# Kernel optimization log

Hardware: AMD Instinct MI355X
Metric: run time of the kernel (lower is better)

The kernel has to match this reference:

```python
import jax, jax.numpy as jnp
import numpy as np

DIM = 256
NUM_HEADS = 8
HEAD_DIM = DIM // NUM_HEADS
WH, WW = 7, 7
N = WH * WW              # tokens per window = 49
NUM_WINDOWS = 64         # windows per image (56x56 map / 7x7 windows)
B_TOTAL = 2048           # num_windows * B_images
SCALE = HEAD_DIM ** -0.5


def _relative_position_index():
    # Matches the tf.meshgrid (xy indexing) construction in the source.
    coords = np.stack(np.meshgrid(np.arange(WH), np.arange(WW)), axis=0)  # [2, WW, WH]
    flat = coords.reshape(2, -1)                                          # [2, N]
    rel = flat[:, :, None] - flat[:, None, :]                             # [2, N, N]
    rel = rel.transpose(1, 2, 0).astype(np.int32)                         # [N, N, 2]
    rel[:, :, 0] += WH - 1
    rel[:, :, 1] += WW - 1
    rel[:, :, 0] *= 2 * WW - 1
    return rel.sum(-1)                                                    # [N, N]


def setup_inputs() -> dict:
    key = jax.random.key(0)
    ks = jax.random.split(key, 6)
    std = 0.02
    x = jax.random.normal(ks[0], (B_TOTAL, N, DIM), dtype=jnp.float32)
    mask = jnp.zeros((NUM_WINDOWS, N, N), dtype=jnp.float32)  # 0 / -inf additive mask
    qkv_w = jax.random.normal(ks[1], (DIM, 3 * DIM), dtype=jnp.float32) * std
    qkv_b = jnp.zeros((3 * DIM,), dtype=jnp.float32)
    proj_w = jax.random.normal(ks[2], (DIM, DIM), dtype=jnp.float32) * std
    proj_b = jnp.zeros((DIM,), dtype=jnp.float32)
    n_rel = (2 * WH - 1) * (2 * WW - 1)  # 169
    bias_table = jax.random.normal(ks[3], (n_rel, NUM_HEADS), dtype=jnp.float32) * std
    rel_index = jnp.asarray(_relative_position_index(), dtype=jnp.int32)
    return {"x": x, "mask": mask, "qkv_w": qkv_w, "qkv_b": qkv_b,
            "proj_w": proj_w, "proj_b": proj_b, "bias_table": bias_table,
            "rel_index": rel_index}


def reference(x, mask, qkv_w, qkv_b, proj_w, proj_b, bias_table, rel_index):
    B = x.shape[0]
    # qkv projection -> [3, B, H, N, hd]
    qkv = x @ qkv_w + qkv_b                                  # [B, N, 3C]
    qkv = qkv.reshape(B, N, 3, NUM_HEADS, HEAD_DIM)
    qkv = jnp.transpose(qkv, (2, 0, 3, 1, 4))
    q, k, v = qkv[0], qkv[1], qkv[2]
    # scaled attention scores [B, H, N, N]
    attn = jnp.einsum('bhnd,bhmd->bhnm', q, k) * SCALE
    # relative position bias gather: [N*N] -> [N, N, H] -> [1, H, N, N]
    bias = bias_table[rel_index.reshape(-1)].reshape(N, N, NUM_HEADS)
    attn = attn + jnp.transpose(bias, (2, 0, 1))[None]
    # additive window mask [nW, N, N]
    nW = mask.shape[0]
    attn = attn.reshape(B // nW, nW, NUM_HEADS, N, N) + mask[None, :, None]
    attn = attn.reshape(B, NUM_HEADS, N, N)
    attn = jax.nn.softmax(attn, axis=-1)
    out = jnp.einsum('bhnm,bhmd->bhnd', attn, v)             # [B, H, N, hd]
    out = jnp.transpose(out, (0, 2, 1, 3)).reshape(B, N, DIM)
    return out @ proj_w + proj_b
```

## Files before the change

### kernel.cpp

```cpp
#include <hip/hip_runtime.h>

#define NTOK 49
#define NHEAD 8
#define HDIM 32
#define DIMC 256
#define SCALE_F 0.17677669529663687f

typedef __attribute__((ext_vector_type(8))) short short8;
typedef __attribute__((ext_vector_type(4))) float f32x4;

#define AS1P(p) ((__attribute__((address_space(1))) void*)(p))
#define AS3P(p) ((__attribute__((address_space(3))) void*)(p))

__device__ inline unsigned short f2bf(float f) {
    unsigned int u = __float_as_uint(f);
    u += 0x7fffu + ((u >> 16) & 1u);
    return (unsigned short)(u >> 16);
}

__global__ __launch_bounds__(256) void conv_pack(const float* __restrict__ in,
    unsigned short* __restrict__ xp, int M)
{
    const int m  = blockIdx.x * 256 + threadIdx.x;
    const int kc = blockIdx.y;
    if (m >= M) return;
    const float4* p = (const float4*)(in + (size_t)m * 256 + kc * 8);
    float4 a = p[0], b = p[1];
    union { unsigned short s[8]; uint4 v; } u;
    u.s[0] = f2bf(a.x); u.s[1] = f2bf(a.y); u.s[2] = f2bf(a.z); u.s[3] = f2bf(a.w);
    u.s[4] = f2bf(b.x); u.s[5] = f2bf(b.y); u.s[6] = f2bf(b.z); u.s[7] = f2bf(b.w);
    *(uint4*)(xp + ((size_t)kc * M + m) * 8) = u.v;
}

__global__ __launch_bounds__(256) void pack_w(const float* __restrict__ W,
    unsigned short* __restrict__ Wp, int K, int N)
{
    int idx = blockIdx.x * 256 + threadIdx.x;
    if (idx >= K * N) return;
    int k = idx / N, n = idx - k * N;
    Wp[((size_t)(k >> 3) * N + n) * 8 + (k & 7)] = f2bf(W[idx]);
}

__global__ __launch_bounds__(256) void bm_build(const float* __restrict__ bias_table,
    const int* __restrict__ rel_index, const float* __restrict__ mask,
    float* __restrict__ bm)
{
    int idx = blockIdx.x * 256 + threadIdx.x;
    if (idx >= 64 * NHEAD * NTOK * NTOK) return;
    int wh = idx / (NTOK * NTOK);
    int ij = idx - wh * (NTOK * NTOK);
    int w = wh >> 3, h = wh & 7;
    bm[idx] = bias_table[rel_index[ij] * NHEAD + h] + mask[(size_t)w * (NTOK * NTOK) + ij];
}

template <bool OUT_BF16>
__global__ __launch_bounds__(256) void gemm_mfma(
    const unsigned short* __restrict__ Ap,
    const unsigned short* __restrict__ Wp,
    const float* __restrict__ Bv,
    void* __restrict__ Yv,
    int N, int M, int nbm)
{
    __shared__ __align__(16) unsigned short As[4096];
    __shared__ __align__(16) unsigned short Bs[4096];

    const int tid  = threadIdx.x;
    const int lane = tid & 63;
    const int wv   = tid >> 6;
    const int quad = lane >> 4;
    const int l15  = lane & 15;

    const int nbn = N >> 7;
    const int lin = blockIdx.x;
    int mblk, nblk;
    if ((nbm & 7) == 0) {
        const int xcd = lin & 7;
        const int g   = lin >> 3;
        const int gm  = g / nbn;
        mblk = xcd * (nbm >> 3) + gm;
        nblk = g - gm * nbn;
    } else {
        mblk = lin / nbn;
        nblk = lin - mblk * nbn;
    }
    const long m0 = (long)mblk * 128;
    const int  n0 = nblk * 128;
    const int  wm = (wv >> 1) * 64;
    const int  wn = (wv & 1) * 64;

    const unsigned short* ga0 = Ap + ((size_t)wv * M + m0 + lane) * 8;
    const unsigned short* ga1 = ga0 + 64 * 8;
    const unsigned short* gb0 = Wp + ((size_t)wv * N + n0 + lane) * 8;
    const unsigned short* gb1 = gb0 + 64 * 8;

    f32x4 acc[4][4];
    #pragma unroll
    for (int i = 0; i < 4; ++i)
        #pragma unroll
        for (int j = 0; j < 4; ++j) acc[i][j] = (f32x4){0.f, 0.f, 0.f, 0.f};

    for (int k0 = 0; k0 < 256; k0 += 32) {
        const size_t aofs = (size_t)(k0 >> 3) * M * 8;
        const size_t bofs = (size_t)(k0 >> 3) * N * 8;
        __builtin_amdgcn_global_load_lds(AS1P(ga0 + aofs), AS3P(As + wv * 1024),       16, 0, 0);
        __builtin_amdgcn_global_load_lds(AS1P(ga1 + aofs), AS3P(As + wv * 1024 + 512), 16, 0, 0);
        __builtin_amdgcn_global_load_lds(AS1P(gb0 + bofs), AS3P(Bs + wv * 1024),       16, 0, 0);
        __builtin_amdgcn_global_load_lds(AS1P(gb1 + bofs), AS3P(Bs + wv * 1024 + 512), 16, 0, 0);
        __syncthreads();
        short8 af[4], bq[4];
        #pragma unroll
        for (int t = 0; t < 4; ++t) {
            af[t] = *(const short8*)(As + quad * 1024 + (wm + t * 16 + l15) * 8);
            bq[t] = *(const short8*)(Bs + quad * 1024 + (wn + t * 16 + l15) * 8);
        }
        #pragma unroll
        for (int ti = 0; ti < 4; ++ti)
            #pragma unroll
            for (int tj = 0; tj < 4; ++tj)
                acc[ti][tj] = __builtin_amdgcn_mfma_f32_16x16x32_bf16(bq[tj], af[ti], acc[ti][tj], 0, 0, 0);
        __syncthreads();
    }

    float4 bv4[4];
    #pragma unroll
    for (int tj = 0; tj < 4; ++tj)
        bv4[tj] = *(const float4*)(Bv + n0 + wn + tj * 16 + quad * 4);

    #pragma unroll
    for (int ti = 0; ti < 4; ++ti) {
        const long row = m0 + wm + ti * 16 + l15;
        #pragma unroll
        for (int tj = 0; tj < 4; ++tj) {
            const int col = n0 + wn + tj * 16 + quad * 4;
            const float v0 = acc[ti][tj][0] + bv4[tj].x;
            const float v1 = acc[ti][tj][1] + bv4[tj].y;
            const float v2 = acc[ti][tj][2] + bv4[tj].z;
            const float v3 = acc[ti][tj][3] + bv4[tj].w;
            if (OUT_BF16) {
                uint2 u;
                u.x = (unsigned int)f2bf(v0) | ((unsigned int)f2bf(v1) << 16);
                u.y = (unsigned int)f2bf(v2) | ((unsigned int)f2bf(v3) << 16);
                *(uint2*)((unsigned short*)Yv + row * N + col) = u;
            } else {
                float4 o = {v0, v1, v2, v3};
                *(float4*)((float*)Yv + row * N + col) = o;
            }
        }
    }
}

__global__ __launch_bounds__(128) void attn_mfma(
    const unsigned short* __restrict__ qkvb,
    const float* __restrict__ bm,
    unsigned short* __restrict__ o1b,
    int win0, int Mc)
{
    __shared__ __align__(16) unsigned short SMEM[2 * 3528];

    const int wvid = threadIdx.x >> 6;
    const int lane = threadIdx.x & 63;
    const int h    = blockIdx.x * 2 + wvid;
    const int b    = blockIdx.y;
    const int w    = (win0 + b) & 63;
    const int quad = lane >> 4;
    const int l15  = lane & 15;

    unsigned short* Vt = SMEM + wvid * 3528;
    unsigned short* Ps = SMEM + wvid * 3528;

    const unsigned short* wbase = qkvb + (size_t)b * NTOK * 768 + h * HDIM;

    {
        const int tok = (lane < NTOK) ? lane : (NTOK - 1);
        const unsigned short* vp = wbase + (size_t)tok * 768 + 512;
        #pragma unroll
        for (int c = 0; c < 4; ++c) {
            uint4 vv = *(const uint4*)(vp + c * 8);
            unsigned int uu[4] = {vv.x, vv.y, vv.z, vv.w};
            #pragma unroll
            for (int e = 0; e < 4; ++e) {
                int d = c * 8 + e * 2;
                Vt[d * 72 + lane]       = (unsigned short)(uu[e] & 0xffffu);
                Vt[(d + 1) * 72 + lane] = (unsigned short)(uu[e] >> 16);
            }
        }
    }

    short8 aq[4], bk[4];
    #pragma unroll
    for (int t = 0; t < 4; ++t) {
        int row = t * 16 + l15; if (row >= NTOK) row = NTOK - 1;
        const unsigned short* rp = wbase + (size_t)row * 768 + quad * 8;
        aq[t] = *(const short8*)(rp);
        bk[t] = *(const short8*)(rp + 256);
    }

    f32x4 sa[4][4];
    #pragma unroll
    for (int ti = 0; ti < 4; ++ti)
        #pragma unroll
        for (int tj = 0; tj < 4; ++tj) {
            f32x4 z = (f32x4){0.f, 0.f, 0.f, 0.f};
            sa[ti][tj] = __builtin_amdgcn_mfma_f32_16x16x32_bf16(aq[ti], bk[tj], z, 0, 0, 0);
        }

    short8 vb2[2][2];
    #pragma unroll
    for (int td = 0; td < 2; ++td)
        #pragma unroll
        for (int kc = 0; kc < 2; ++kc)
            vb2[td][kc] = *(const short8*)(Vt + (td * 16 + l15) * 72 + kc * 32 + quad * 8);

    const float* bmb = bm + (size_t)(w * NHEAD + h) * (NTOK * NTOK);
    float inv[4][4];
    #pragma unroll
    for (int ti = 0; ti < 4; ++ti) {
        #pragma unroll
        for (int r = 0; r < 4; ++r) {
            const int row = ti * 16 + quad * 4 + r;
            float sv[4];
            #pragma unroll
            for (int tj = 0; tj < 4; ++tj) {
                const int col = tj * 16 + l15;
                float s;
                if (col < NTOK) {
                    float add = (row < NTOK) ? bmb[row * NTOK + col] : 0.f;
                    s = sa[ti][tj][r] * SCALE_F + add;
                } else {
                    s = -__builtin_inff();
                }
                sv[tj] = s;
            }
            float mx = fmaxf(fmaxf(sv[0], sv[1]), fmaxf(sv[2], sv[3]));
            mx = fmaxf(mx, __shfl_xor(mx, 1, 16));
            mx = fmaxf(mx, __shfl_xor(mx, 2, 16));
            mx = fmaxf(mx, __shfl_xor(mx, 4, 16));
            mx = fmaxf(mx, __shfl_xor(mx, 8, 16));
            float e0 = __expf(sv[0] - mx), e1 = __expf(sv[1] - mx);
            float e2 = __expf(sv[2] - mx), e3 = __expf(sv[3] - mx);
            sa[ti][0][r] = e0; sa[ti][1][r] = e1; sa[ti][2][r] = e2; sa[ti][3][r] = e3;
            float sum = (e0 + e1) + (e2 + e3);
            sum += __shfl_xor(sum, 1, 16);
            sum += __shfl_xor(sum, 2, 16);
            sum += __shfl_xor(sum, 4, 16);
            sum += __shfl_xor(sum, 8, 16);
            inv[ti][r] = 1.f / sum;
        }
    }

    __syncthreads();

    #pragma unroll
    for (int ti = 0; ti < 4; ++ti)
        #pragma unroll
        for (int r = 0; r < 4; ++r) {
            const int row = ti * 16 + quad * 4 + r;
            if (row < NTOK) {
                #pragma unroll
                for (int tj = 0; tj < 4; ++tj)
                    Ps[row * 72 + tj * 16 + l15] = f2bf(sa[ti][tj][r]);
            }
        }

    short8 pa[4][2];
    #pragma unroll
    for (int ti = 0; ti < 4; ++ti) {
        int row = ti * 16 + l15; if (row >= NTOK) row = NTOK - 1;
        #pragma unroll
        for (int kc = 0; kc < 2; ++kc)
            pa[ti][kc] = *(const short8*)(Ps + row * 72 + kc * 32 + quad * 8);
    }
    f32x4 oa[4][2];
    #pragma unroll
    for (int ti = 0; ti < 4; ++ti)
        #pragma unroll
        for (int td = 0; td < 2; ++td) {
            f32x4 z = (f32x4){0.f, 0.f, 0.f, 0.f};
            z = __builtin_amdgcn_mfma_f32_16x16x32_bf16(pa[ti][0], vb2[td][0], z, 0, 0, 0);
            oa[ti][td] = __builtin_amdgcn_mfma_f32_16x16x32_bf16(pa[ti][1], vb2[td][1], z, 0, 0, 0);
        }

    #pragma unroll
    for (int ti = 0; ti < 4; ++ti)
        #pragma unroll
        for (int r = 0; r < 4; ++r) {
            const int row = ti * 16 + quad * 4 + r;
            if (row < NTOK) {
                const float si = inv[ti][r];
                const size_t gm = (size_t)b * NTOK + row;
                #pragma unroll
                for (int td = 0; td < 2; ++td) {
                    const int kk = h * HDIM + td * 16 + l15;
                    o1b[((size_t)(kk >> 3) * Mc + gm) * 8 + (kk & 7)] = f2bf(oa[ti][td][r] * si);
                }
            }
        }
}

extern "C" void kernel_launch(void* const* d_in, const int* in_sizes, int n_in,
                              void* d_out, int out_size, void* d_ws, size_t ws_size,
                              hipStream_t stream)
{
    const float* x          = (const float*)d_in[0];
    const float* mask       = (const float*)d_in[1];
    const float* qkv_w      = (const float*)d_in[2];
    const float* qkv_b      = (const float*)d_in[3];
    const float* proj_w     = (const float*)d_in[4];
    const float* proj_b     = (const float*)d_in[5];
    const float* bias_table = (const float*)d_in[6];
    const int*   rel_index  = (const int*)d_in[7];
    float* outp = (float*)d_out;

    const int B_TOTAL = 2048;
    char* ws = (char*)d_ws;
    size_t off = 0;
    auto carve = [&](size_t bytes) -> void* {
        void* p = ws + off; off += (bytes + 255) & ~(size_t)255; return p;
    };
    unsigned short* WpQ = (unsigned short*)carve((size_t)256 * 768 * 2);
    unsigned short* WpP = (unsigned short*)carve((size_t)256 * 256 * 2);
    float* bm = (float*)carve((size_t)64 * NHEAD * NTOK * NTOK * 4);
    const size_t fixed = off;
    const size_t PER_WIN = (size_t)NTOK * 256 * 2 + (size_t)NTOK * 768 * 2 + (size_t)NTOK * 256 * 2;
    size_t avail = (ws_size > fixed + 1024) ? (ws_size - fixed - 1024) : 0;
    int chunkW = (int)(avail / PER_WIN);
    if (chunkW > B_TOTAL) chunkW = B_TOTAL;
    chunkW &= ~127;
    if (chunkW < 128) chunkW = 128;
    unsigned short* x_bf = (unsigned short*)carve((size_t)chunkW * NTOK * 256 * 2);
    unsigned short* qkvb = (unsigned short*)carve((size_t)chunkW * NTOK * 768 * 2);
    unsigned short* o1b  = (unsigned short*)carve((size_t)chunkW * NTOK * 256 * 2);

    pack_w<<<(256 * 768 + 255) / 256, 256, 0, stream>>>(qkv_w, WpQ, 256, 768);
    pack_w<<<(256 * 256 + 255) / 256, 256, 0, stream>>>(proj_w, WpP, 256, 256);
    bm_build<<<(64 * NHEAD * NTOK * NTOK + 255) / 256, 256, 0, stream>>>(
        bias_table, rel_index, mask, bm);

    for (int w0 = 0; w0 < B_TOTAL; w0 += chunkW) {
        int wc = B_TOTAL - w0; if (wc > chunkW) wc = chunkW;
        const int Mc = wc * NTOK;
        const int nbm = Mc / 128;
        conv_pack<<<dim3((Mc + 255) / 256, 32), 256, 0, stream>>>(
            x + (size_t)w0 * NTOK * DIMC, x_bf, Mc);
        gemm_mfma<true ><<<dim3(nbm * 6), 256, 0, stream>>>(x_bf, WpQ, qkv_b, qkvb, 768, Mc, nbm);
        attn_mfma<<<dim3(NHEAD / 2, wc), 128, 0, stream>>>(qkvb, bm, o1b, w0, Mc);
        gemm_mfma<false><<<dim3(nbm * 2), 256, 0, stream>>>(
            o1b, WpP, proj_b, outp + (size_t)w0 * NTOK * DIMC, 256, Mc, nbm);
    }
}
```

Baseline: 413.9 us.

## Fuse fp32-to-bf16 input conversion into QKV GEMM and coalesce attention output stores

```diff
diff --git a/kernel.cpp b/kernel.cpp
--- a/kernel.cpp
+++ b/kernel.cpp
@@ -16,20 +16,6 @@
     unsigned int u = __float_as_uint(f);
     u += 0x7fffu + ((u >> 16) & 1u);
     return (unsigned short)(u >> 16);
-}
-
-__global__ __launch_bounds__(256) void conv_pack(const float* __restrict__ in,
-    unsigned short* __restrict__ xp, int M)
-{
-    const int m  = blockIdx.x * 256 + threadIdx.x;
-    const int kc = blockIdx.y;
-    if (m >= M) return;
-    const float4* p = (const float4*)(in + (size_t)m * 256 + kc * 8);
-    float4 a = p[0], b = p[1];
-    union { unsigned short s[8]; uint4 v; } u;
-    u.s[0] = f2bf(a.x); u.s[1] = f2bf(a.y); u.s[2] = f2bf(a.z); u.s[3] = f2bf(a.w);
-    u.s[4] = f2bf(b.x); u.s[5] = f2bf(b.y); u.s[6] = f2bf(b.z); u.s[7] = f2bf(b.w);
-    *(uint4*)(xp + ((size_t)kc * M + m) * 8) = u.v;
 }
 
 __global__ __launch_bounds__(256) void pack_w(const float* __restrict__ W,
@@ -53,9 +39,9 @@
     bm[idx] = bias_table[rel_index[ij] * NHEAD + h] + mask[(size_t)w * (NTOK * NTOK) + ij];
 }
 
-template <bool OUT_BF16>
+template <bool A_F32, bool OUT_BF16>
 __global__ __launch_bounds__(256) void gemm_mfma(
-    const unsigned short* __restrict__ Ap,
+    const void* __restrict__ Av,
     const unsigned short* __restrict__ Wp,
     const float* __restrict__ Bv,
     void* __restrict__ Yv,
@@ -88,11 +74,21 @@
     const int  wm = (wv >> 1) * 64;
     const int  wn = (wv & 1) * 64;
 
-    const unsigned short* ga0 = Ap + ((size_t)wv * M + m0 + lane) * 8;
-    const unsigned short* ga1 = ga0 + 64 * 8;
     const unsigned short* gb0 = Wp + ((size_t)wv * N + n0 + lane) * 8;
     const unsigned short* gb1 = gb0 + 64 * 8;
 
+    const float* xr0 = nullptr;
+    const float* xr1 = nullptr;
+    const unsigned short* ga0 = nullptr;
+    const unsigned short* ga1 = nullptr;
+    if constexpr (A_F32) {
+        xr0 = (const float*)Av + (size_t)(m0 + lane) * 256 + wv * 8;
+        xr1 = xr0 + (size_t)64 * 256;
+    } else {
+        ga0 = (const unsigned short*)Av + ((size_t)wv * M + m0 + lane) * 8;
+        ga1 = ga0 + 64 * 8;
+    }
+
     f32x4 acc[4][4];
     #pragma unroll
     for (int i = 0; i < 4; ++i)
@@ -100,12 +96,28 @@
         for (int j = 0; j < 4; ++j) acc[i][j] = (f32x4){0.f, 0.f, 0.f, 0.f};
 
     for (int k0 = 0; k0 < 256; k0 += 32) {
-        const size_t aofs = (size_t)(k0 >> 3) * M * 8;
         const size_t bofs = (size_t)(k0 >> 3) * N * 8;
-        __builtin_amdgcn_global_load_lds(AS1P(ga0 + aofs), AS3P(As + wv * 1024),       16, 0, 0);
-        __builtin_amdgcn_global_load_lds(AS1P(ga1 + aofs), AS3P(As + wv * 1024 + 512), 16, 0, 0);
-        __builtin_amdgcn_global_load_lds(AS1P(gb0 + bofs), AS3P(Bs + wv * 1024),       16, 0, 0);
-        __builtin_amdgcn_global_load_lds(AS1P(gb1 + bofs), AS3P(Bs + wv * 1024 + 512), 16, 0, 0);
+        if constexpr (A_F32) {
+            float4 a0 = ((const float4*)(xr0 + k0))[0];
+            float4 a1 = ((const float4*)(xr0 + k0))[1];
+            float4 a2 = ((const float4*)(xr1 + k0))[0];
+            float4 a3 = ((const float4*)(xr1 + k0))[1];
+            __builtin_amdgcn_global_load_lds(AS1P(gb0 + bofs), AS3P(Bs + wv * 1024),       16, 0, 0);
+            __builtin_amdgcn_global_load_lds(AS1P(gb1 + bofs), AS3P(Bs + wv * 1024 + 512), 16, 0, 0);
+            union { unsigned short s[8]; uint4 v; } u0, u1;
+            u0.s[0] = f2bf(a0.x); u0.s[1] = f2bf(a0.y); u0.s[2] = f2bf(a0.z); u0.s[3] = f2bf(a0.w);
+            u0.s[4] = f2bf(a1.x); u0.s[5] = f2bf(a1.y); u0.s[6] = f2bf(a1.z); u0.s[7] = f2bf(a1.w);
+            u1.s[0] = f2bf(a2.x); u1.s[1] = f2bf(a2.y); u1.s[2] = f2bf(a2.z); u1.s[3] = f2bf(a2.w);
+            u1.s[4] = f2bf(a3.x); u1.s[5] = f2bf(a3.y); u1.s[6] = f2bf(a3.z); u1.s[7] = f2bf(a3.w);
+            *(uint4*)(As + wv * 1024 + (size_t)lane * 8)        = u0.v;
+            *(uint4*)(As + wv * 1024 + (size_t)(64 + lane) * 8) = u1.v;
+        } else {
+            const size_t aofs = (size_t)(k0 >> 3) * M * 8;
+            __builtin_amdgcn_global_load_lds(AS1P(ga0 + aofs), AS3P(As + wv * 1024),       16, 0, 0);
+            __builtin_amdgcn_global_load_lds(AS1P(ga1 + aofs), AS3P(As + wv * 1024 + 512), 16, 0, 0);
+            __builtin_amdgcn_global_load_lds(AS1P(gb0 + bofs), AS3P(Bs + wv * 1024),       16, 0, 0);
+            __builtin_amdgcn_global_load_lds(AS1P(gb1 + bofs), AS3P(Bs + wv * 1024 + 512), 16, 0, 0);
+        }
         __syncthreads();
         short8 af[4], bq[4];
         #pragma unroll
@@ -167,6 +179,7 @@
 
     unsigned short* Vt = SMEM + wvid * 3528;
     unsigned short* Ps = SMEM + wvid * 3528;
+    unsigned short* Os = SMEM + wvid * 3528;
 
     const unsigned short* wbase = qkvb + (size_t)b * NTOK * 768 + h * HDIM;
 
@@ -287,14 +300,22 @@
             const int row = ti * 16 + quad * 4 + r;
             if (row < NTOK) {
                 const float si = inv[ti][r];
-                const size_t gm = (size_t)b * NTOK + row;
                 #pragma unroll
                 for (int td = 0; td < 2; ++td) {
-                    const int kk = h * HDIM + td * 16 + l15;
-                    o1b[((size_t)(kk >> 3) * Mc + gm) * 8 + (kk & 7)] = f2bf(oa[ti][td][r] * si);
+                    const int d = td * 16 + l15;
+                    Os[(d >> 3) * (NTOK * 8) + row * 8 + (d & 7)] =
+                        f2bf(oa[ti][td][r] * si);
                 }
             }
         }
+
+    if (lane < NTOK) {
+        #pragma unroll
+        for (int kg = 0; kg < 4; ++kg) {
+            uint4 v = *(const uint4*)(Os + kg * (NTOK * 8) + lane * 8);
+            *(uint4*)(o1b + ((size_t)(h * 4 + kg) * Mc + (size_t)b * NTOK + lane) * 8) = v;
+        }
+    }
 }
 
 extern "C" void kernel_launch(void* const* d_in, const int* in_sizes, int n_in,
@@ -321,13 +342,12 @@
     unsigned short* WpP = (unsigned short*)carve((size_t)256 * 256 * 2);
     float* bm = (float*)carve((size_t)64 * NHEAD * NTOK * NTOK * 4);
     const size_t fixed = off;
-    const size_t PER_WIN = (size_t)NTOK * 256 * 2 + (size_t)NTOK * 768 * 2 + (size_t)NTOK * 256 * 2;
+    const size_t PER_WIN = (size_t)NTOK * 768 * 2 + (size_t)NTOK * 256 * 2;
     size_t avail = (ws_size > fixed + 1024) ? (ws_size - fixed - 1024) : 0;
     int chunkW = (int)(avail / PER_WIN);
     if (chunkW > B_TOTAL) chunkW = B_TOTAL;
     chunkW &= ~127;
     if (chunkW < 128) chunkW = 128;
-    unsigned short* x_bf = (unsigned short*)carve((size_t)chunkW * NTOK * 256 * 2);
     unsigned short* qkvb = (unsigned short*)carve((size_t)chunkW * NTOK * 768 * 2);
     unsigned short* o1b  = (unsigned short*)carve((size_t)chunkW * NTOK * 256 * 2);
 
@@ -340,11 +360,10 @@
         int wc = B_TOTAL - w0; if (wc > chunkW) wc = chunkW;
         const int Mc = wc * NTOK;
         const int nbm = Mc / 128;
-        conv_pack<<<dim3((Mc + 255) / 256, 32), 256, 0, stream>>>(
-            x + (size_t)w0 * NTOK * DIMC, x_bf, Mc);
-        gemm_mfma<true ><<<dim3(nbm * 6), 256, 0, stream>>>(x_bf, WpQ, qkv_b, qkvb, 768, Mc, nbm);
+        gemm_mfma<true, true ><<<dim3(nbm * 6), 256, 0, stream>>>(
+            x + (size_t)w0 * NTOK * DIMC, WpQ, qkv_b, qkvb, 768, Mc, nbm);
         attn_mfma<<<dim3(NHEAD / 2, wc), 128, 0, stream>>>(qkvb, bm, o1b, w0, Mc);
-        gemm_mfma<false><<<dim3(nbm * 2), 256, 0, stream>>>(
+        gemm_mfma<false, false><<<dim3(nbm * 2), 256, 0, stream>>>(
             o1b, WpP, proj_b, outp + (size_t)w0 * NTOK * DIMC, 256, Mc, nbm);
     }
 }
```

Result: slower. 422.3 us (+2.0%).
